# Performance work log

Measured on AMD Instinct MI355X. Metric: run time of the kernel, lower is better.

Reference implementation:

```python
import jax
import jax.numpy as jnp
from jax import lax
import numpy as np

V, E, H, H2, C, B, L = 50000, 256, 256, 128, 12, 64, 512
START, STOP = 10, 11
IMPOSSIBLE = -10000.0


def setup_inputs() -> dict:
    key = jax.random.key(0)
    ks = jax.random.split(key, 30)
    rn = lambda k, s, sc=0.1: jax.random.normal(k, s, jnp.float32) * sc
    d = {}
    d["sentence"] = jax.random.randint(ks[0], (B, L), 0, V)
    d["masks"] = jnp.ones((B, L), jnp.float32)
    d["emb_table"] = rn(ks[1], (V, E))
    i = 2
    for layer, din in ((1, E), (2, H)):
        for dr in ("f", "r"):
            d["w_ih_%s%d" % (dr, layer)] = rn(ks[i], (4 * H2, din)); i += 1
            d["w_hh_%s%d" % (dr, layer)] = rn(ks[i], (4 * H2, H2)); i += 1
            d["b_ih_%s%d" % (dr, layer)] = rn(ks[i], (4 * H2,)); i += 1
            d["b_hh_%s%d" % (dr, layer)] = rn(ks[i], (4 * H2,)); i += 1
    d["w_out"] = rn(ks[i], (C, H)); i += 1
    d["b_out"] = rn(ks[i], (C,)); i += 1
    tr = jax.random.normal(ks[i], (C, C), jnp.float32); i += 1
    d["transitions"] = tr.at[START, :].set(IMPOSSIBLE).at[:, STOP].set(IMPOSSIBLE)
    for nm in ("h0_1", "c0_1", "h0_2", "c0_2"):
        d[nm] = rn(ks[i], (2, B, H2), 1.0); i += 1
    return d


def _lstm_dir(x, h0, c0, w_ih, w_hh, b_ih, b_hh, reverse):
    # x: [L, B, Din]; PyTorch LSTM gate order: i, f, g, o
    b = b_ih + b_hh
    def step(carry, xt):
        h, c = carry
        g = xt @ w_ih.T + h @ w_hh.T + b  # [B, 4*H2]
        i, f, gg, o = jnp.split(g, 4, axis=-1)
        c = jax.nn.sigmoid(f) * c + jax.nn.sigmoid(i) * jnp.tanh(gg)
        h = jax.nn.sigmoid(o) * jnp.tanh(c)
        return (h, c), h
    _, hs = lax.scan(step, (h0, c0), x, reverse=reverse)
    return hs  # [L, B, H2]


def _bilstm(x, h0, c0, pf, pr):
    hf = _lstm_dir(x, h0[0], c0[0], *pf, reverse=False)
    hr = _lstm_dir(x, h0[1], c0[1], *pr, reverse=True)
    return jnp.concatenate([hf, hr], axis=-1)  # [L, B, H]


def reference(sentence, masks, emb_table,
              w_ih_f1, w_hh_f1, b_ih_f1, b_hh_f1, w_ih_r1, w_hh_r1, b_ih_r1, b_hh_r1,
              w_ih_f2, w_hh_f2, b_ih_f2, b_hh_f2, w_ih_r2, w_hh_r2, b_ih_r2, b_hh_r2,
              w_out, b_out, transitions, h0_1, c0_1, h0_2, c0_2):
    Bb, Ll = sentence.shape
    # faithful to the original: embedding output is .view()'d (reshaped), not transposed
    embeds = emb_table[sentence].reshape(Ll, Bb, -1)  # [L, B, E]
    out1 = _bilstm(embeds, h0_1, c0_1,
                   (w_ih_f1, w_hh_f1, b_ih_f1, b_hh_f1),
                   (w_ih_r1, w_hh_r1, b_ih_r1, b_hh_r1))
    out2 = _bilstm(out1, h0_2, c0_2,
                   (w_ih_f2, w_hh_f2, b_ih_f2, b_hh_f2),
                   (w_ih_r2, w_hh_r2, b_ih_r2, b_hh_r2))
    feats = out2.reshape(Bb, Ll, -1) @ w_out.T + b_out  # [B, L, C]
    Cc = feats.shape[-1]

    # Viterbi forward pass over time
    init = jnp.full((Bb, Cc), IMPOSSIBLE, jnp.float32).at[:, START].set(0.0)
    def vstep(ms, inp):
        emit, m = inp  # [B, C], [B]
        acc = ms[:, None, :] + transitions[None]  # [B, C_to, C_from]
        bp = jnp.argmax(acc, axis=-1)             # [B, C]
        sc = jnp.max(acc, axis=-1) + emit
        mm = m[:, None]
        return sc * mm + ms * (1.0 - mm), bp
    final, bps = lax.scan(vstep, init, (feats.transpose(1, 0, 2), masks.T))  # bps: [L, B, C]
    final = final + transitions[STOP]
    best_score = final.max(axis=-1)        # [B]
    best_tag = jnp.argmax(final, axis=-1)  # [B]

    # vectorized backtrace: tag[len-1] = best_tag; tag[t] = bps[t+1][tag[t+1]]
    lengths = masks.sum(axis=1).astype(jnp.int32)  # [B]
    bps_next = jnp.concatenate([bps[1:], bps[-1:]], axis=0)  # bps_next[t] = bps[t+1]
    ts = jnp.arange(Ll)
    def bstep(cur, inp):
        t, bpn = inp  # bpn: [B, C]
        nxt = jnp.take_along_axis(bpn, cur[:, None], axis=1)[:, 0]
        new = jnp.where(t >= lengths - 1, best_tag, nxt)
        return new, new
    _, path = lax.scan(bstep, best_tag, (ts, bps_next), reverse=True)  # [L, B]
    path = path.T  # [B, L]
    path = jnp.where(ts[None, :] < lengths[:, None], path, 0)
    return best_score, path
```

## Files before the change

kernel.cpp:

```cpp
#include <hip/hip_runtime.h>
#include <math.h>

#define VSZ   50000
#define EDIM  256
#define HDIM  256
#define H2D   128
#define NCLS  12
#define NB    64
#define NL    512
#define G4    512
#define NNC   1024
#define MM    32768
#define START_TAG 10
#define STOP_TAG  11
#define IMPOSSIBLE -10000.0f

__device__ __forceinline__ float sigmoidf_(float x) {
    return 1.0f / (1.0f + expf(-x));
}

template <bool GATHER>
__global__ __launch_bounds__(256)
void gemm_gates(const float* __restrict__ A,
                const int*   __restrict__ gidx,
                const float* __restrict__ wf,
                const float* __restrict__ wr,
                const float* __restrict__ bihf, const float* __restrict__ bhhf,
                const float* __restrict__ bihr, const float* __restrict__ bhhr,
                float* __restrict__ out)
{
    __shared__ __align__(16) float As[32][132];
    __shared__ __align__(16) float Bs[32][132];

    const int tid = threadIdx.x;
    const int n0  = blockIdx.x * 128;
    const int m0  = blockIdx.y * 128;
    const int ty  = tid >> 4;
    const int tx  = tid & 15;

    float acc[8][8];
#pragma unroll
    for (int i = 0; i < 8; ++i)
#pragma unroll
        for (int j = 0; j < 8; ++j) acc[i][j] = 0.0f;

    const bool  fwdside = (n0 < 512);
    const float* wsrc   = fwdside ? wf : wr;
    const int    nbase  = fwdside ? n0 : (n0 - 512);

    int srcA[4];
#pragma unroll
    for (int it = 0; it < 4; ++it) {
        int li  = tid + it * 256;
        int row = m0 + (li >> 3);
        srcA[it] = GATHER ? gidx[row] : row;
    }

    for (int kt = 0; kt < 8; ++kt) {
#pragma unroll
        for (int it = 0; it < 4; ++it) {
            int li = tid + it * 256;
            int r  = li >> 3;
            int c4 = li & 7;
            float4 v = ((const float4*)A)[(size_t)srcA[it] * 64 + kt * 8 + c4];
            As[c4 * 4 + 0][r] = v.x;
            As[c4 * 4 + 1][r] = v.y;
            As[c4 * 4 + 2][r] = v.z;
            As[c4 * 4 + 3][r] = v.w;
        }
#pragma unroll
        for (int it = 0; it < 4; ++it) {
            int li = tid + it * 256;
            int r  = li >> 3;
            int c4 = li & 7;
            float4 v = ((const float4*)wsrc)[(size_t)(nbase + r) * 64 + kt * 8 + c4];
            Bs[c4 * 4 + 0][r] = v.x;
            Bs[c4 * 4 + 1][r] = v.y;
            Bs[c4 * 4 + 2][r] = v.z;
            Bs[c4 * 4 + 3][r] = v.w;
        }
        __syncthreads();

#pragma unroll
        for (int k = 0; k < 32; ++k) {
            float a[8], b[8];
            *(float4*)&a[0] = *(const float4*)&As[k][ty * 8];
            *(float4*)&a[4] = *(const float4*)&As[k][ty * 8 + 4];
            *(float4*)&b[0] = *(const float4*)&Bs[k][tx * 8];
            *(float4*)&b[4] = *(const float4*)&Bs[k][tx * 8 + 4];
#pragma unroll
            for (int i = 0; i < 8; ++i)
#pragma unroll
                for (int j = 0; j < 8; ++j)
                    acc[i][j] = fmaf(a[i], b[j], acc[i][j]);
        }
        __syncthreads();
    }

    float bias[8];
#pragma unroll
    for (int j = 0; j < 8; ++j) {
        int gn = n0 + tx * 8 + j;
        bias[j] = fwdside ? (bihf[gn] + bhhf[gn]) : (bihr[gn - 512] + bhhr[gn - 512]);
    }
#pragma unroll
    for (int i = 0; i < 8; ++i) {
        int m = m0 + ty * 8 + i;
        float4 s0, s1;
        s0.x = acc[i][0] + bias[0]; s0.y = acc[i][1] + bias[1];
        s0.z = acc[i][2] + bias[2]; s0.w = acc[i][3] + bias[3];
        s1.x = acc[i][4] + bias[4]; s1.y = acc[i][5] + bias[5];
        s1.z = acc[i][6] + bias[6]; s1.w = acc[i][7] + bias[7];
        float4* op = (float4*)(out + (size_t)m * NNC + n0 + tx * 8);
        op[0] = s0;
        op[1] = s1;
    }
}

__global__ __launch_bounds__(512, 2)
void lstm_rec(const float* __restrict__ gx,
              const float* __restrict__ whf,
              const float* __restrict__ whr,
              const float* __restrict__ h0,
              const float* __restrict__ c0,
              float* __restrict__ out)
{
    __shared__ __align__(16) float h_lds[H2D];
    __shared__ __align__(16) float gates[G4];

    const int j   = threadIdx.x;
    const int dir = blockIdx.x >> 6;
    const int bb  = blockIdx.x & 63;
    const float* W = dir ? whr : whf;

    float w[H2D];
#pragma unroll
    for (int k4 = 0; k4 < 32; ++k4) {
        float4 v = ((const float4*)W)[(size_t)j * 32 + k4];
        w[4 * k4 + 0] = v.x; w[4 * k4 + 1] = v.y;
        w[4 * k4 + 2] = v.z; w[4 * k4 + 3] = v.w;
    }

    float creg = 0.0f;
    if (j < H2D) {
        h_lds[j] = h0[dir * (NB * H2D) + bb * H2D + j];
        creg     = c0[dir * (NB * H2D) + bb * H2D + j];
    }
    __syncthreads();

    const int chunk = j >> 7;
    const float4* h4 = (const float4*)h_lds;

    for (int ti = 0; ti < NL; ++ti) {
        const int t = dir ? (NL - 1 - ti) : ti;
        const size_t m = (size_t)t * NB + bb;

        const float gxv = gx[m * NNC + dir * 512 + j];

        float dot = 0.0f;
#pragma unroll
        for (int k4 = 0; k4 < 32; ++k4) {
            float4 hv = h4[k4];
            dot = fmaf(w[4 * k4 + 0], hv.x, dot);
            dot = fmaf(w[4 * k4 + 1], hv.y, dot);
            dot = fmaf(w[4 * k4 + 2], hv.z, dot);
            dot = fmaf(w[4 * k4 + 3], hv.w, dot);
        }
        const float pre = dot + gxv;
        const float act = (chunk == 2) ? tanhf(pre) : sigmoidf_(pre);
        gates[j] = act;
        __syncthreads();

        if (j < H2D) {
            const float ig = gates[j];
            const float fg = gates[j + 128];
            const float gg = gates[j + 256];
            const float og = gates[j + 384];
            creg = fg * creg + ig * gg;
            const float hnew = og * tanhf(creg);
            h_lds[j] = hnew;
            out[m * HDIM + dir * H2D + j] = hnew;
        }
        __syncthreads();
    }
}

__global__ __launch_bounds__(256)
void feats_kernel(const float* __restrict__ out2,
                  const float* __restrict__ w_out,
                  const float* __restrict__ b_out,
                  float* __restrict__ feats)
{
    __shared__ __align__(16) float wl[NCLS * HDIM];
    const int tid = threadIdx.x;
#pragma unroll
    for (int i = 0; i < NCLS; ++i) wl[tid + i * 256] = w_out[tid + i * 256];
    __syncthreads();

    const int m = blockIdx.x * 256 + tid;
    float acc[NCLS];
#pragma unroll
    for (int c = 0; c < NCLS; ++c) acc[c] = 0.0f;

    const float4* x4 = (const float4*)out2 + (size_t)m * 64;
    const float4* w4 = (const float4*)wl;
    for (int k4 = 0; k4 < 64; ++k4) {
        float4 x = x4[k4];
#pragma unroll
        for (int c = 0; c < NCLS; ++c) {
            float4 wv = w4[c * 64 + k4];
            acc[c] = fmaf(x.x, wv.x, acc[c]);
            acc[c] = fmaf(x.y, wv.y, acc[c]);
            acc[c] = fmaf(x.z, wv.z, acc[c]);
            acc[c] = fmaf(x.w, wv.w, acc[c]);
        }
    }
#pragma unroll
    for (int c = 0; c < NCLS; ++c)
        feats[(size_t)m * NCLS + c] = acc[c] + b_out[c];
}

__global__ __launch_bounds__(64)
void viterbi_fwd(const float* __restrict__ feats,
                 const float* __restrict__ masks,
                 const float* __restrict__ trans,
                 float* __restrict__ best_score,
                 unsigned char* __restrict__ bps,
                 int* __restrict__ best_tag)
{
    const int b    = blockIdx.x;
    const int lane = threadIdx.x;

    float tr[NCLS];
#pragma unroll
    for (int jj = 0; jj < NCLS; ++jj)
        tr[jj] = (lane < NCLS) ? trans[lane * NCLS + jj] : 0.0f;

    float msv = (lane == START_TAG) ? 0.0f : IMPOSSIBLE;

    for (int t = 0; t < NL; ++t) {
        const float emit = (lane < NCLS) ? feats[((size_t)b * NL + t) * NCLS + lane] : 0.0f;
        const float mt   = masks[b * NL + t];

        float best = -3.4e38f;
        int   bj   = 0;
#pragma unroll
        for (int jj = 0; jj < NCLS; ++jj) {
            float msj = __shfl(msv, jj);
            float v   = msj + tr[jj];
            if (v > best) { best = v; bj = jj; }
        }
        const float sc = best + emit;
        msv = mt * sc + (1.0f - mt) * msv;
        if (lane < NCLS)
            bps[((size_t)t * NB + b) * NCLS + lane] = (unsigned char)bj;
    }

    const float fin = (lane < NCLS) ? (msv + trans[STOP_TAG * NCLS + lane]) : -3.4e38f;
    float bv = -3.4e38f;
    int   bt = 0;
#pragma unroll
    for (int jj = 0; jj < NCLS; ++jj) {
        float v = __shfl(fin, jj);
        if (v > bv) { bv = v; bt = jj; }
    }
    if (lane == 0) {
        best_score[b] = bv;
        best_tag[b]   = bt;
    }
}

__global__ __launch_bounds__(64)
void backtrace(const unsigned char* __restrict__ bps,
               const int* __restrict__ best_tag,
               const float* __restrict__ masks,
               float* __restrict__ path_out)
{
    const int b = threadIdx.x;
    float s = 0.0f;
    for (int t = 0; t < NL; ++t) s += masks[b * NL + t];
    const int len  = (int)(s + 0.5f);
    const int btag = best_tag[b];

    int cur = btag;
    for (int t = NL - 1; t >= 0; --t) {
        const int tb  = (t == NL - 1) ? (NL - 1) : (t + 1);
        const int nxt = bps[((size_t)tb * NB + b) * NCLS + cur];
        const int val = (t >= len - 1) ? btag : nxt;
        cur = val;
        path_out[(size_t)b * NL + t] = (t < len) ? (float)val : 0.0f;
    }
}

extern "C" void kernel_launch(void* const* d_in, const int* in_sizes, int n_in,
                              void* d_out, int out_size, void* d_ws, size_t ws_size,
                              hipStream_t stream)
{
    const int*   sentence = (const int*)  d_in[0];
    const float* masks    = (const float*)d_in[1];
    const float* emb      = (const float*)d_in[2];
    const float* w_ih_f1  = (const float*)d_in[3];
    const float* w_hh_f1  = (const float*)d_in[4];
    const float* b_ih_f1  = (const float*)d_in[5];
    const float* b_hh_f1  = (const float*)d_in[6];
    const float* w_ih_r1  = (const float*)d_in[7];
    const float* w_hh_r1  = (const float*)d_in[8];
    const float* b_ih_r1  = (const float*)d_in[9];
    const float* b_hh_r1  = (const float*)d_in[10];
    const float* w_ih_f2  = (const float*)d_in[11];
    const float* w_hh_f2  = (const float*)d_in[12];
    const float* b_ih_f2  = (const float*)d_in[13];
    const float* b_hh_f2  = (const float*)d_in[14];
    const float* w_ih_r2  = (const float*)d_in[15];
    const float* w_hh_r2  = (const float*)d_in[16];
    const float* b_ih_r2  = (const float*)d_in[17];
    const float* b_hh_r2  = (const float*)d_in[18];
    const float* w_out    = (const float*)d_in[19];
    const float* b_out    = (const float*)d_in[20];
    const float* trans    = (const float*)d_in[21];
    const float* h0_1     = (const float*)d_in[22];
    const float* c0_1     = (const float*)d_in[23];
    const float* h0_2     = (const float*)d_in[24];
    const float* c0_2     = (const float*)d_in[25];

    float* gx    = (float*)d_ws;
    float* out1  = gx   + (size_t)MM * NNC;
    float* out2  = out1 + (size_t)MM * HDIM;
    float* feats = out2 + (size_t)MM * HDIM;
    int*   btag  = (int*)(feats + (size_t)MM * NCLS);
    unsigned char* bps = (unsigned char*)(btag + 64);

    dim3 gemm_grid(NNC / 128, MM / 128);

    gemm_gates<true><<<gemm_grid, 256, 0, stream>>>(
        emb, sentence, w_ih_f1, w_ih_r1, b_ih_f1, b_hh_f1, b_ih_r1, b_hh_r1, gx);
    lstm_rec<<<128, 512, 0, stream>>>(gx, w_hh_f1, w_hh_r1, h0_1, c0_1, out1);

    gemm_gates<false><<<gemm_grid, 256, 0, stream>>>(
        out1, nullptr, w_ih_f2, w_ih_r2, b_ih_f2, b_hh_f2, b_ih_r2, b_hh_r2, gx);
    lstm_rec<<<128, 512, 0, stream>>>(gx, w_hh_f2, w_hh_r2, h0_2, c0_2, out2);

    feats_kernel<<<MM / 256, 256, 0, stream>>>(out2, w_out, b_out, feats);
    viterbi_fwd<<<NB, 64, 0, stream>>>(feats, masks, trans, (float*)d_out, bps, btag);
    backtrace<<<1, 64, 0, stream>>>(bps, btag, masks, (float*)d_out + 64);
}
```

Measured before the change: 1.858 ms.

## Halve LSTM recurrence block size with two gates per thread and remap GEMM lanes

The recurrent LSTM kernel now runs 256 threads per block, and each thread computes two gate rows (256 weights in registers). Threads below 128 keep the input and cell gates locally and exchange only the forget and output gates through shared memory, which shrinks shared-memory traffic and synchronization width per timestep. Split accumulators shorten the FMA dependency chains. The gate GEMM also remaps threads to a wave-tiled layout (2x2 waves, each covering 64x64) to change the shared-memory read pattern. The cost is higher register pressure (256 weight registers per thread) and fewer waves to hide latency on the sequential critical path.

New measurement: 2.586 ms. 39.2% more time.

```diff
diff --git a/kernel.cpp b/kernel.cpp
--- a/kernel.cpp
+++ b/kernel.cpp
@@ -35,8 +35,15 @@
     const int tid = threadIdx.x;
     const int n0  = blockIdx.x * 128;
     const int m0  = blockIdx.y * 128;
-    const int ty  = tid >> 4;
-    const int tx  = tid & 15;
+
+    const int w    = tid >> 6;
+    const int lane = tid & 63;
+    const int wm   = w >> 1;
+    const int wn   = w & 1;
+    const int am   = lane >> 3;
+    const int bn   = lane & 7;
+    const int ma   = wm * 64 + am * 8;
+    const int nb   = wn * 64 + bn * 8;
 
     float acc[8][8];
 #pragma unroll
@@ -44,9 +51,9 @@
 #pragma unroll
         for (int j = 0; j < 8; ++j) acc[i][j] = 0.0f;
 
-    const bool  fwdside = (n0 < 512);
-    const float* wsrc   = fwdside ? wf : wr;
-    const int    nbase  = fwdside ? n0 : (n0 - 512);
+    const bool   fwdside = (n0 < 512);
+    const float* wsrc    = fwdside ? wf : wr;
+    const int    nbase   = fwdside ? n0 : (n0 - 512);
 
     int srcA[4];
 #pragma unroll
@@ -84,10 +91,10 @@
 #pragma unroll
         for (int k = 0; k < 32; ++k) {
             float a[8], b[8];
-            *(float4*)&a[0] = *(const float4*)&As[k][ty * 8];
-            *(float4*)&a[4] = *(const float4*)&As[k][ty * 8 + 4];
-            *(float4*)&b[0] = *(const float4*)&Bs[k][tx * 8];
-            *(float4*)&b[4] = *(const float4*)&Bs[k][tx * 8 + 4];
+            *(float4*)&a[0] = *(const float4*)&As[k][ma];
+            *(float4*)&a[4] = *(const float4*)&As[k][ma + 4];
+            *(float4*)&b[0] = *(const float4*)&Bs[k][nb];
+            *(float4*)&b[4] = *(const float4*)&Bs[k][nb + 4];
 #pragma unroll
             for (int i = 0; i < 8; ++i)
 #pragma unroll
@@ -100,24 +107,24 @@
     float bias[8];
 #pragma unroll
     for (int j = 0; j < 8; ++j) {
-        int gn = n0 + tx * 8 + j;
+        int gn = n0 + nb + j;
         bias[j] = fwdside ? (bihf[gn] + bhhf[gn]) : (bihr[gn - 512] + bhhr[gn - 512]);
     }
 #pragma unroll
     for (int i = 0; i < 8; ++i) {
-        int m = m0 + ty * 8 + i;
+        int m = m0 + ma + i;
         float4 s0, s1;
         s0.x = acc[i][0] + bias[0]; s0.y = acc[i][1] + bias[1];
         s0.z = acc[i][2] + bias[2]; s0.w = acc[i][3] + bias[3];
         s1.x = acc[i][4] + bias[4]; s1.y = acc[i][5] + bias[5];
         s1.z = acc[i][6] + bias[6]; s1.w = acc[i][7] + bias[7];
-        float4* op = (float4*)(out + (size_t)m * NNC + n0 + tx * 8);
+        float4* op = (float4*)(out + (size_t)m * NNC + n0 + nb);
         op[0] = s0;
         op[1] = s1;
     }
 }
 
-__global__ __launch_bounds__(512, 2)
+__global__ __launch_bounds__(256, 1)
 void lstm_rec(const float* __restrict__ gx,
               const float* __restrict__ whf,
               const float* __restrict__ whr,
@@ -126,19 +133,25 @@
               float* __restrict__ out)
 {
     __shared__ __align__(16) float h_lds[H2D];
-    __shared__ __align__(16) float gates[G4];
+    __shared__ __align__(16) float fo[256];
 
     const int j   = threadIdx.x;
     const int dir = blockIdx.x >> 6;
     const int bb  = blockIdx.x & 63;
     const float* W = dir ? whr : whf;
 
-    float w[H2D];
+    const int g0 = j;
+    const int g1 = j + 256;
+
+    float w0[H2D], w1[H2D];
 #pragma unroll
     for (int k4 = 0; k4 < 32; ++k4) {
-        float4 v = ((const float4*)W)[(size_t)j * 32 + k4];
-        w[4 * k4 + 0] = v.x; w[4 * k4 + 1] = v.y;
-        w[4 * k4 + 2] = v.z; w[4 * k4 + 3] = v.w;
+        float4 v0 = ((const float4*)W)[(size_t)g0 * 32 + k4];
+        float4 v1 = ((const float4*)W)[(size_t)g1 * 32 + k4];
+        w0[4 * k4 + 0] = v0.x; w0[4 * k4 + 1] = v0.y;
+        w0[4 * k4 + 2] = v0.z; w0[4 * k4 + 3] = v0.w;
+        w1[4 * k4 + 0] = v1.x; w1[4 * k4 + 1] = v1.y;
+        w1[4 * k4 + 2] = v1.z; w1[4 * k4 + 3] = v1.w;
     }
 
     float creg = 0.0f;
@@ -148,35 +161,46 @@
     }
     __syncthreads();
 
-    const int chunk = j >> 7;
     const float4* h4 = (const float4*)h_lds;
+    const bool low = (j < H2D);
 
     for (int ti = 0; ti < NL; ++ti) {
         const int t = dir ? (NL - 1 - ti) : ti;
         const size_t m = (size_t)t * NB + bb;
 
-        const float gxv = gx[m * NNC + dir * 512 + j];
-
-        float dot = 0.0f;
+        const float gx0 = gx[m * NNC + dir * 512 + g0];
+        const float gx1 = gx[m * NNC + dir * 512 + g1];
+
+        float d00 = 0.f, d01 = 0.f, d02 = 0.f, d03 = 0.f;
+        float d10 = 0.f, d11 = 0.f, d12 = 0.f, d13 = 0.f;
 #pragma unroll
         for (int k4 = 0; k4 < 32; ++k4) {
-            float4 hv = h4[k4];
-            dot = fmaf(w[4 * k4 + 0], hv.x, dot);
-            dot = fmaf(w[4 * k4 + 1], hv.y, dot);
-            dot = fmaf(w[4 * k4 + 2], hv.z, dot);
-            dot = fmaf(w[4 * k4 + 3], hv.w, dot);
-        }
-        const float pre = dot + gxv;
-        const float act = (chunk == 2) ? tanhf(pre) : sigmoidf_(pre);
-        gates[j] = act;
+            const float4 hv = h4[k4];
+            d00 = fmaf(w0[4 * k4 + 0], hv.x, d00);
+            d01 = fmaf(w0[4 * k4 + 1], hv.y, d01);
+            d02 = fmaf(w0[4 * k4 + 2], hv.z, d02);
+            d03 = fmaf(w0[4 * k4 + 3], hv.w, d03);
+            d10 = fmaf(w1[4 * k4 + 0], hv.x, d10);
+            d11 = fmaf(w1[4 * k4 + 1], hv.y, d11);
+            d12 = fmaf(w1[4 * k4 + 2], hv.z, d12);
+            d13 = fmaf(w1[4 * k4 + 3], hv.w, d13);
+        }
+        const float pre0 = ((d00 + d01) + (d02 + d03)) + gx0;
+        const float pre1 = ((d10 + d11) + (d12 + d13)) + gx1;
+
+        const float act0 = sigmoidf_(pre0);
+        const float act1 = low ? tanhf(pre1) : sigmoidf_(pre1);
+
+        if (!low) {
+            fo[j - 128] = act0;
+            fo[j]       = act1;
+        }
         __syncthreads();
 
-        if (j < H2D) {
-            const float ig = gates[j];
-            const float fg = gates[j + 128];
-            const float gg = gates[j + 256];
-            const float og = gates[j + 384];
-            creg = fg * creg + ig * gg;
+        if (low) {
+            const float fg = fo[j];
+            const float og = fo[j + 128];
+            creg = fg * creg + act0 * act1;
             const float hnew = og * tanhf(creg);
             h_lds[j] = hnew;
             out[m * HDIM + dir * H2D + j] = hnew;
@@ -334,11 +358,11 @@
 
     gemm_gates<true><<<gemm_grid, 256, 0, stream>>>(
         emb, sentence, w_ih_f1, w_ih_r1, b_ih_f1, b_hh_f1, b_ih_r1, b_hh_r1, gx);
-    lstm_rec<<<128, 512, 0, stream>>>(gx, w_hh_f1, w_hh_r1, h0_1, c0_1, out1);
+    lstm_rec<<<128, 256, 0, stream>>>(gx, w_hh_f1, w_hh_r1, h0_1, c0_1, out1);
 
     gemm_gates<false><<<gemm_grid, 256, 0, stream>>>(
         out1, nullptr, w_ih_f2, w_ih_r2, b_ih_f2, b_hh_f2, b_ih_r2, b_hh_r2, gx);
-    lstm_rec<<<128, 512, 0, stream>>>(gx, w_hh_f2, w_hh_r2, h0_2, c0_2, out2);
+    lstm_rec<<<128, 256, 0, stream>>>(gx, w_hh_f2, w_hh_r2, h0_2, c0_2, out2);
 
     feats_kernel<<<MM / 256, 256, 0, stream>>>(out2, w_out, b_out, feats);
     viterbi_fwd<<<NB, 64, 0, stream>>>(feats, masks, trans, (float*)d_out, bps, btag);
```
